# Kernel optimization log

Measured on AMD Instinct MI355X. Metric: run time of the kernel, lower is better.

The kernel has to match this reference:

```python
import jax, jax.numpy as jnp
import numpy as np

MUL = 16          # multiplicity of every irrep block
N = 131072        # number of nodes

# orthonormal traceless-symmetric 3x3 basis, divided by sqrt(5).
_s = 1.0 / np.sqrt(2.0)
_M = np.zeros((5, 3, 3), dtype=np.float32)
_M[0, 0, 1] = _M[0, 1, 0] = _s
_M[1, 0, 2] = _M[1, 2, 0] = _s
_M[2, 1, 2] = _M[2, 2, 1] = _s
_M[3, 0, 0] = _s; _M[3, 1, 1] = -_s
_M[4] = np.diag([-1.0, -1.0, 2.0]).astype(np.float32) / np.sqrt(6.0)
C112 = jnp.asarray(np.transpose(_M, (1, 2, 0)) / np.sqrt(5.0))  # (3,3,5)

# e3nn TensorProduct normalization: irrep_normalization='component'
# (alpha = 2l_out+1), path_normalization='element' (divide by sum of
# mul_u*mul_v over paths into the same output irrep). 0e output receives
# two paths -> 2*MUL^2; 1o and 2e each receive one path -> MUL^2.
A000 = float(np.sqrt(1.0 / (2.0 * MUL * MUL)))                    # 0e x 0e -> 0e (w3j = 1)
A110 = float(np.sqrt(1.0 / (2.0 * MUL * MUL)) / np.sqrt(3.0))     # 1o x 1o -> 0e (w3j = d_ij/sqrt(3))
A101 = float(np.sqrt(3.0 / (MUL * MUL)) / np.sqrt(3.0))           # 1o x 0e -> 1o (w3j = d_ik/sqrt(3))
A112 = float(np.sqrt(5.0 / (MUL * MUL)))                          # 1o x 1o -> 2e


def setup_inputs() -> dict:
    key = jax.random.key(0)
    ks = jax.random.split(key, 6)
    f = lambda k, s: jax.random.normal(k, s, dtype=jnp.float32)
    return {
        "node_feats": f(ks[0], (N, 4 * MUL)),
        "node_messages": f(ks[1], (N, 4 * MUL)),
        "w000": f(ks[2], (MUL, MUL, MUL)),
        "w101": f(ks[3], (MUL, MUL, MUL)),
        "w110": f(ks[4], (MUL, MUL, MUL)),
        "w112": f(ks[5], (MUL, MUL, MUL)),
    }


def _tensor_square(x, w000, w101, w110, w112):
    """e3nn o3.TensorSquare('16x0e+16x1o', '16x0e+16x1o+16x2e') with 'uvw' weighted paths."""
    n = x.shape[0]
    x0 = x[:, :MUL]                          # (n, u)     l=0 block
    x1 = x[:, MUL:].reshape(n, MUL, 3)       # (n, u, i)  l=1 block (mul-major)

    # --- 0e output ---
    out0 = A000 * jnp.einsum('uvw,nu,nv->nw', w000, x0, x0)
    out0 = out0 + A110 * jnp.einsum('uvw,nui,nvi->nw', w110, x1, x1)

    # --- 1o output ---
    out1 = A101 * jnp.einsum('uvw,nuk,nv->nwk', w101, x1, x0)

    # --- 2e output (staged to keep intermediates small) ---
    t1 = jnp.einsum('nvj,ijk->nvik', x1, C112)        # (n, v, i, 5)
    t = jnp.einsum('nui,nvik->nuvk', x1, t1)          # (n, u, v, 5)
    out2 = A112 * jnp.einsum('uvw,nuvk->nwk', w112, t)

    return jnp.concatenate(
        [out0, out1.reshape(n, 3 * MUL), out2.reshape(n, 5 * MUL)], axis=1
    )  # (n, 144)


def reference(node_feats, node_messages, w000, w101, w110, w112):
    # SimpleNodeBlock: sum all nodewise tensors, then tensor square.
    return _tensor_square(node_feats + node_messages, w000, w101, w110, w112)
```

## Files before the change

### kernel.cpp

```cpp
#include <hip/hip_runtime.h>

#define MUL 16
#define NPAIR 136
#define NPB 16
#define SSTR 40
#define NTILE 23

typedef __bf16 bf16x8 __attribute__((ext_vector_type(8)));
typedef __bf16 bf16x2 __attribute__((ext_vector_type(2)));
typedef float  f32x4  __attribute__((ext_vector_type(4)));

__global__ void prep_weights(const float* __restrict__ w000,
                             const float* __restrict__ w101,
                             const float* __restrict__ w110,
                             const float* __restrict__ w112,
                             __bf16* __restrict__ wt) {
    const int tid = threadIdx.x;
    for (int i = tid; i < NTILE * 64; i += 256) {
        bf16x8 z = {};
        ((bf16x8*)wt)[i] = z;
    }
    __syncthreads();

    const float A000   = 0.044194173824159216f;
    const float A110   = 0.025515518153991442f;
    const float A101   = 0.0625f;
    const float A112C1 = 0.044194173824159216f;

    for (int idx = tid; idx < NPAIR * MUL; idx += 256) {
        int p = idx / MUL, w = idx % MUL;
        int u = 0, rem = p;
        while (rem >= MUL - u) { rem -= MUL - u; ++u; }
        int v = u + rem;

        int uv = (u * MUL + v) * MUL + w;
        int vu = (v * MUL + u) * MUL + w;
        float f000, f110, f112, fuv, fvu;
        if (u == v) {
            f000 = A000   * w000[uv];
            f110 = A110   * w110[uv];
            f112 = A112C1 * w112[uv];
            fuv  = A101   * w101[uv];
            fvu  = 0.f;
        } else {
            f000 = A000   * (w000[uv] + w000[vu]);
            f110 = A110   * (w110[uv] + w110[vu]);
            f112 = A112C1 * (w112[uv] + w112[vu]);
            fuv  = A101   * w101[uv];
            fvu  = A101   * w101[vu];
        }
        auto put = [&](int T, int kit, float val) {
            int lanei = ((kit >> 3) << 4) + w;
            wt[(T * 64 + lanei) * 8 + (kit & 7)] = (__bf16)val;
        };
        int k = 2 * p, k2 = 2 * p + 1;
        put(k >> 5,        k & 31,  f000);
        put(k2 >> 5,       k2 & 31, f110);
        put(9 + (k >> 5),  k & 31,  fuv);
        put(9 + (k2 >> 5), k2 & 31, fvu);
        put(18 + (p >> 5), p & 31,  f112);
    }
}

__launch_bounds__(256, 4)
__global__ void tsq_kernel(const float* __restrict__ feats,
                           const float* __restrict__ msgs,
                           const __bf16* __restrict__ wtiles,
                           float* __restrict__ out) {
    __shared__ float  xq[NPB * 68];
    __shared__ int    UVs[NPAIR];
    __shared__ __bf16 sbuf[2][NPB * SSTR];
    __shared__ __bf16 pqbuf[2][3][NPB * SSTR];
    __shared__ __bf16 tbuf[2][5][NPB * SSTR];

    const int tid = threadIdx.x;
    const long long blockNode = (long long)blockIdx.x * NPB;

    if (tid < NPAIR) {
        int u = 0, rem = tid;
        while (rem >= MUL - u) { rem -= MUL - u; ++u; }
        UVs[tid] = u | ((u + rem) << 16);
    }
    {
        int nd = tid >> 4, v = tid & 15;
        const float* fp = feats + (blockNode + nd) * 64;
        const float* mp = msgs  + (blockNode + nd) * 64;
        float4 qd;
        qd.x = fp[v]          + mp[v];
        qd.y = fp[16 + 3 * v] + mp[16 + 3 * v];
        qd.z = fp[17 + 3 * v] + mp[17 + 3 * v];
        qd.w = fp[18 + 3 * v] + mp[18 + 3 * v];
        *(float4*)&xq[nd * 68 + 4 * v] = qd;
    }
    __syncthreads();

    const float SQ3  = 1.7320508075688772f;
    const float ISQ3 = 0.5773502691896258f;
    const int nd = tid & 15, pi = tid >> 4;

    auto computeSP = [&](int c, int b) {
        int P = 16 * c + pi;
        int o = nd * SSTR + 2 * pi;
        if (P < NPAIR) {
            int uvp = UVs[P];
            int u = uvp & 0xffff, v = uvp >> 16;
            float4 xu = *(const float4*)&xq[nd * 68 + 4 * u];
            float4 xv = *(const float4*)&xq[nd * 68 + 4 * v];
            float s0 = xu.x * xv.x;
            float s1 = xu.y * xv.y + xu.z * xv.z + xu.w * xv.w;
            *(bf16x2*)&sbuf[b][o]      = (bf16x2){(__bf16)s0, (__bf16)s1};
            *(bf16x2*)&pqbuf[b][0][o]  = (bf16x2){(__bf16)(xu.y * xv.x), (__bf16)(xv.y * xu.x)};
            *(bf16x2*)&pqbuf[b][1][o]  = (bf16x2){(__bf16)(xu.z * xv.x), (__bf16)(xv.z * xu.x)};
            *(bf16x2*)&pqbuf[b][2][o]  = (bf16x2){(__bf16)(xu.w * xv.x), (__bf16)(xv.w * xu.x)};
        } else {
            bf16x2 z = {};
            *(bf16x2*)&sbuf[b][o]     = z;
            *(bf16x2*)&pqbuf[b][0][o] = z;
            *(bf16x2*)&pqbuf[b][1][o] = z;
            *(bf16x2*)&pqbuf[b][2][o] = z;
        }
    };

    auto computeT = [&](int c, int b) {
        float tf[5][2];
#pragma unroll
        for (int e = 0; e < 2; ++e) {
            int P = 32 * c + 2 * pi + e;
            if (P < NPAIR) {
                int uvp = UVs[P];
                int u = uvp & 0xffff, v = uvp >> 16;
                float4 xu = *(const float4*)&xq[nd * 68 + 4 * u];
                float4 xv = *(const float4*)&xq[nd * 68 + 4 * v];
                float o00 = xu.y * xv.y, o01 = xu.y * xv.z, o02 = xu.y * xv.w;
                float o10 = xu.z * xv.y, o11 = xu.z * xv.z, o12 = xu.z * xv.w;
                float o20 = xu.w * xv.y, o21 = xu.w * xv.z, o22 = xu.w * xv.w;
                float s1 = (o00 + o11) + o22;
                tf[0][e] = o01 + o10;
                tf[1][e] = o02 + o20;
                tf[2][e] = o12 + o21;
                tf[3][e] = o00 - o11;
                tf[4][e] = SQ3 * o22 - ISQ3 * s1;
            } else {
#pragma unroll
                for (int k = 0; k < 5; ++k) tf[k][e] = 0.f;
            }
        }
        int o = nd * SSTR + 2 * pi;
#pragma unroll
        for (int k = 0; k < 5; ++k)
            *(bf16x2*)&tbuf[b][k][o] = (bf16x2){(__bf16)tf[k][0], (__bf16)tf[k][1]};
    };

    const int lane = tid & 63;
    const int wid  = __builtin_amdgcn_readfirstlane(tid >> 6);
    const int m = lane & 15, q = lane >> 4;
    const int kk = wid - 1;
    const bf16x8* wb = (const bf16x8*)wtiles;

    f32x4 accA = {0.f, 0.f, 0.f, 0.f};
    f32x4 accB = {0.f, 0.f, 0.f, 0.f};
    f32x4 accC = {0.f, 0.f, 0.f, 0.f};

    computeSP(0, 0);
    __syncthreads();
    for (int c = 0; c < 9; ++c) {
        if (c < 8) computeSP(c + 1, (c + 1) & 1);
        int b = c & 1;
        if (wid == 0) {
            accA = __builtin_amdgcn_mfma_f32_16x16x32_bf16(
                *(const bf16x8*)&sbuf[b][m * SSTR + 8 * q],
                wb[c * 64 + lane], accA, 0, 0, 0);
        } else {
            accA = __builtin_amdgcn_mfma_f32_16x16x32_bf16(
                *(const bf16x8*)&pqbuf[b][kk][m * SSTR + 8 * q],
                wb[(9 + c) * 64 + lane], accA, 0, 0, 0);
        }
        __syncthreads();
    }

    computeT(0, 0);
    __syncthreads();
    for (int c = 0; c < 5; ++c) {
        if (c < 4) computeT(c + 1, (c + 1) & 1);
        int b = c & 1;
        bf16x8 bt = wb[(18 + c) * 64 + lane];
        if (wid == 0) {
            accB = __builtin_amdgcn_mfma_f32_16x16x32_bf16(
                *(const bf16x8*)&tbuf[b][3][m * SSTR + 8 * q], bt, accB, 0, 0, 0);
            accC = __builtin_amdgcn_mfma_f32_16x16x32_bf16(
                *(const bf16x8*)&tbuf[b][4][m * SSTR + 8 * q], bt, accC, 0, 0, 0);
        } else {
            accB = __builtin_amdgcn_mfma_f32_16x16x32_bf16(
                *(const bf16x8*)&tbuf[b][kk][m * SSTR + 8 * q], bt, accB, 0, 0, 0);
        }
        __syncthreads();
    }

    const int w = m;
    if (wid == 0) {
#pragma unroll
        for (int r = 0; r < 4; ++r) {
            int ndo = q * 4 + r;
            float* ob = out + (blockNode + ndo) * 144;
            ob[w]              = accA[r];
            ob[64 + 5 * w + 3] = accB[r];
            ob[64 + 5 * w + 4] = accC[r];
        }
    } else {
#pragma unroll
        for (int r = 0; r < 4; ++r) {
            int ndo = q * 4 + r;
            float* ob = out + (blockNode + ndo) * 144;
            ob[16 + 3 * w + kk] = accA[r];
            ob[64 + 5 * w + kk] = accB[r];
        }
    }
}

extern "C" void kernel_launch(void* const* d_in, const int* in_sizes, int n_in,
                              void* d_out, int out_size, void* d_ws, size_t ws_size,
                              hipStream_t stream) {
    const float* feats = (const float*)d_in[0];
    const float* msgs  = (const float*)d_in[1];
    const float* w000  = (const float*)d_in[2];
    const float* w101  = (const float*)d_in[3];
    const float* w110  = (const float*)d_in[4];
    const float* w112  = (const float*)d_in[5];
    __bf16* wt = (__bf16*)d_ws;
    float* out = (float*)d_out;

    const int n = in_sizes[0] / (4 * MUL);

    prep_weights<<<1, 256, 0, stream>>>(w000, w101, w110, w112, wt);
    tsq_kernel<<<n / NPB, 256, 0, stream>>>(feats, msgs, wt, out);
}
```

Baseline: 191.7 us.

## Build MFMA A-fragments in registers per wave, dropping LDS staging and barriers

```diff
diff --git a/kernel.cpp b/kernel.cpp
--- a/kernel.cpp
+++ b/kernel.cpp
@@ -2,218 +2,221 @@
 
 #define MUL 16
 #define NPAIR 136
-#define NPB 16
-#define SSTR 40
-#define NTILE 23
+#define NTILE 25
 
 typedef __bf16 bf16x8 __attribute__((ext_vector_type(8)));
-typedef __bf16 bf16x2 __attribute__((ext_vector_type(2)));
 typedef float  f32x4  __attribute__((ext_vector_type(4)));
+
+__device__ __forceinline__ void uv_of(int p, int& u, int& v) {
+    if (p >= NPAIR) { u = 0; v = 0; return; }
+    int uu = 0, rem = p;
+    while (rem >= MUL - uu) { rem -= MUL - uu; ++uu; }
+    u = uu; v = uu + rem;
+}
 
 __global__ void prep_weights(const float* __restrict__ w000,
                              const float* __restrict__ w101,
                              const float* __restrict__ w110,
                              const float* __restrict__ w112,
                              __bf16* __restrict__ wt) {
-    const int tid = threadIdx.x;
-    for (int i = tid; i < NTILE * 64; i += 256) {
-        bf16x8 z = {};
-        ((bf16x8*)wt)[i] = z;
-    }
-    __syncthreads();
+    const int gid = blockIdx.x * 256 + threadIdx.x;
+    if (gid >= NTILE * 64) return;
+    const int T = gid >> 6, lane = gid & 63;
+    const int q = lane >> 4, w = lane & 15;
 
     const float A000   = 0.044194173824159216f;
     const float A110   = 0.025515518153991442f;
     const float A101   = 0.0625f;
     const float A112C1 = 0.044194173824159216f;
 
-    for (int idx = tid; idx < NPAIR * MUL; idx += 256) {
-        int p = idx / MUL, w = idx % MUL;
-        int u = 0, rem = p;
-        while (rem >= MUL - u) { rem -= MUL - u; ++u; }
-        int v = u + rem;
-
-        int uv = (u * MUL + v) * MUL + w;
-        int vu = (v * MUL + u) * MUL + w;
-        float f000, f110, f112, fuv, fvu;
-        if (u == v) {
-            f000 = A000   * w000[uv];
-            f110 = A110   * w110[uv];
-            f112 = A112C1 * w112[uv];
-            fuv  = A101   * w101[uv];
-            fvu  = 0.f;
-        } else {
-            f000 = A000   * (w000[uv] + w000[vu]);
-            f110 = A110   * (w110[uv] + w110[vu]);
-            f112 = A112C1 * (w112[uv] + w112[vu]);
-            fuv  = A101   * w101[uv];
-            fvu  = A101   * w101[vu];
-        }
-        auto put = [&](int T, int kit, float val) {
-            int lanei = ((kit >> 3) << 4) + w;
-            wt[(T * 64 + lanei) * 8 + (kit & 7)] = (__bf16)val;
-        };
-        int k = 2 * p, k2 = 2 * p + 1;
-        put(k >> 5,        k & 31,  f000);
-        put(k2 >> 5,       k2 & 31, f110);
-        put(9 + (k >> 5),  k & 31,  fuv);
-        put(9 + (k2 >> 5), k2 & 31, fvu);
-        put(18 + (p >> 5), p & 31,  f112);
-    }
-}
-
-__launch_bounds__(256, 4)
+    bf16x8 frag = {};
+    if (T < 10) {
+        const int c = T >> 1, b = T & 1;
+#pragma unroll
+        for (int i = 0; i < 4; ++i) {
+            const int p = 32 * c + 8 * q + 4 * b + i;
+            if (p < NPAIR) {
+                int u, v; uv_of(p, u, v);
+                const int uvw = (u * MUL + v) * MUL + w;
+                const int vuw = (v * MUL + u) * MUL + w;
+                float f000, f110;
+                if (u == v) { f000 = A000 * w000[uvw]; f110 = A110 * w110[uvw]; }
+                else        { f000 = A000 * (w000[uvw] + w000[vuw]);
+                              f110 = A110 * (w110[uvw] + w110[vuw]); }
+                frag[2 * i]     = (__bf16)f000;
+                frag[2 * i + 1] = (__bf16)f110;
+            }
+        }
+    } else if (T < 20) {
+        const int c = (T - 10) >> 1, b = (T - 10) & 1;
+#pragma unroll
+        for (int i = 0; i < 4; ++i) {
+            const int p = 32 * c + 8 * q + 4 * b + i;
+            if (p < NPAIR) {
+                int u, v; uv_of(p, u, v);
+                const int uvw = (u * MUL + v) * MUL + w;
+                const int vuw = (v * MUL + u) * MUL + w;
+                frag[2 * i]     = (__bf16)(A101 * w101[uvw]);
+                frag[2 * i + 1] = (__bf16)((u == v) ? 0.f : A101 * w101[vuw]);
+            }
+        }
+    } else {
+        const int c = T - 20;
+#pragma unroll
+        for (int e = 0; e < 8; ++e) {
+            const int p = 32 * c + 8 * q + e;
+            if (p < NPAIR) {
+                int u, v; uv_of(p, u, v);
+                const int uvw = (u * MUL + v) * MUL + w;
+                const int vuw = (v * MUL + u) * MUL + w;
+                const float f112 = (u == v) ? A112C1 * w112[uvw]
+                                            : A112C1 * (w112[uvw] + w112[vuw]);
+                frag[e] = (__bf16)f112;
+            }
+        }
+    }
+    ((bf16x8*)wt)[T * 64 + lane] = frag;
+}
+
+#define SQ3f  1.7320508075688772f
+#define ISQ3f 0.5773502691896258f
+
+template<int E>
+__device__ __forceinline__ void pair_feats(int d, const float* __restrict__ xrow,
+        bf16x8& fS, bf16x8& f0, bf16x8& f1, bf16x8& f2,
+        bf16x8& t0, bf16x8& t1, bf16x8& t2, bf16x8& t3, bf16x8& t4) {
+    constexpr int sh = (E & 1) * 16;
+    const int u = (d >> sh) & 0xff;
+    const int v = (d >> (sh + 8)) & 0xff;
+    const float4 xu = *(const float4*)(xrow + 4 * u);
+    const float4 xv = *(const float4*)(xrow + 4 * v);
+    const float o00 = xu.y * xv.y, o01 = xu.y * xv.z, o02 = xu.y * xv.w;
+    const float o10 = xu.z * xv.y, o11 = xu.z * xv.z, o12 = xu.z * xv.w;
+    const float o20 = xu.w * xv.y, o21 = xu.w * xv.z, o22 = xu.w * xv.w;
+    const float s1 = (o00 + o11) + o22;
+    constexpr int s2 = (E & 3) * 2;
+    fS[s2]     = (__bf16)(xu.x * xv.x);
+    fS[s2 + 1] = (__bf16)s1;
+    f0[s2]     = (__bf16)(xu.y * xv.x);  f0[s2 + 1] = (__bf16)(xv.y * xu.x);
+    f1[s2]     = (__bf16)(xu.z * xv.x);  f1[s2 + 1] = (__bf16)(xv.z * xu.x);
+    f2[s2]     = (__bf16)(xu.w * xv.x);  f2[s2 + 1] = (__bf16)(xv.w * xu.x);
+    t0[E] = (__bf16)(o01 + o10);
+    t1[E] = (__bf16)(o02 + o20);
+    t2[E] = (__bf16)(o12 + o21);
+    t3[E] = (__bf16)(o00 - o11);
+    t4[E] = (__bf16)(SQ3f * o22 - ISQ3f * s1);
+}
+
+__launch_bounds__(256, 3)
 __global__ void tsq_kernel(const float* __restrict__ feats,
                            const float* __restrict__ msgs,
                            const __bf16* __restrict__ wtiles,
                            float* __restrict__ out) {
-    __shared__ float  xq[NPB * 68];
-    __shared__ int    UVs[NPAIR];
-    __shared__ __bf16 sbuf[2][NPB * SSTR];
-    __shared__ __bf16 pqbuf[2][3][NPB * SSTR];
-    __shared__ __bf16 tbuf[2][5][NPB * SSTR];
+    __shared__ __align__(16) float xq[64 * 68];
+    __shared__ __align__(16) int   uvt[80];
 
     const int tid = threadIdx.x;
-    const long long blockNode = (long long)blockIdx.x * NPB;
-
-    if (tid < NPAIR) {
-        int u = 0, rem = tid;
-        while (rem >= MUL - u) { rem -= MUL - u; ++u; }
-        UVs[tid] = u | ((u + rem) << 16);
-    }
+    const long long blockNode = (long long)blockIdx.x * 64;
+
+    if (tid < 80) {
+        int u0, v0, u1, v1;
+        uv_of(2 * tid,     u0, v0);
+        uv_of(2 * tid + 1, u1, v1);
+        uvt[tid] = u0 | (v0 << 8) | (u1 << 16) | (v1 << 24);
+    }
+
     {
-        int nd = tid >> 4, v = tid & 15;
-        const float* fp = feats + (blockNode + nd) * 64;
-        const float* mp = msgs  + (blockNode + nd) * 64;
-        float4 qd;
-        qd.x = fp[v]          + mp[v];
-        qd.y = fp[16 + 3 * v] + mp[16 + 3 * v];
-        qd.z = fp[17 + 3 * v] + mp[17 + 3 * v];
-        qd.w = fp[18 + 3 * v] + mp[18 + 3 * v];
-        *(float4*)&xq[nd * 68 + 4 * v] = qd;
+        const float4* f4p = (const float4*)(feats + blockNode * 64);
+        const float4* m4p = (const float4*)(msgs  + blockNode * 64);
+#pragma unroll
+        for (int r = 0; r < 4; ++r) {
+            const int li = r * 256 + tid;
+            const int nd = li >> 4, f4 = li & 15;
+            const float4 a = f4p[li];
+            const float4 b = m4p[li];
+            const float vals[4] = {a.x + b.x, a.y + b.y, a.z + b.z, a.w + b.w};
+#pragma unroll
+            for (int jj = 0; jj < 4; ++jj) {
+                const int f = 4 * f4 + jj;
+                int dst;
+                if (f < 16) dst = nd * 68 + 4 * f;
+                else {
+                    const int g = f - 16;
+                    const int v3 = (g * 171) >> 9;
+                    dst = nd * 68 + 4 * v3 + 1 + (g - 3 * v3);
+                }
+                xq[dst] = vals[jj];
+            }
+        }
     }
     __syncthreads();
 
-    const float SQ3  = 1.7320508075688772f;
-    const float ISQ3 = 0.5773502691896258f;
-    const int nd = tid & 15, pi = tid >> 4;
-
-    auto computeSP = [&](int c, int b) {
-        int P = 16 * c + pi;
-        int o = nd * SSTR + 2 * pi;
-        if (P < NPAIR) {
-            int uvp = UVs[P];
-            int u = uvp & 0xffff, v = uvp >> 16;
-            float4 xu = *(const float4*)&xq[nd * 68 + 4 * u];
-            float4 xv = *(const float4*)&xq[nd * 68 + 4 * v];
-            float s0 = xu.x * xv.x;
-            float s1 = xu.y * xv.y + xu.z * xv.z + xu.w * xv.w;
-            *(bf16x2*)&sbuf[b][o]      = (bf16x2){(__bf16)s0, (__bf16)s1};
-            *(bf16x2*)&pqbuf[b][0][o]  = (bf16x2){(__bf16)(xu.y * xv.x), (__bf16)(xv.y * xu.x)};
-            *(bf16x2*)&pqbuf[b][1][o]  = (bf16x2){(__bf16)(xu.z * xv.x), (__bf16)(xv.z * xu.x)};
-            *(bf16x2*)&pqbuf[b][2][o]  = (bf16x2){(__bf16)(xu.w * xv.x), (__bf16)(xv.w * xu.x)};
-        } else {
-            bf16x2 z = {};
-            *(bf16x2*)&sbuf[b][o]     = z;
-            *(bf16x2*)&pqbuf[b][0][o] = z;
-            *(bf16x2*)&pqbuf[b][1][o] = z;
-            *(bf16x2*)&pqbuf[b][2][o] = z;
-        }
-    };
-
-    auto computeT = [&](int c, int b) {
-        float tf[5][2];
-#pragma unroll
-        for (int e = 0; e < 2; ++e) {
-            int P = 32 * c + 2 * pi + e;
-            if (P < NPAIR) {
-                int uvp = UVs[P];
-                int u = uvp & 0xffff, v = uvp >> 16;
-                float4 xu = *(const float4*)&xq[nd * 68 + 4 * u];
-                float4 xv = *(const float4*)&xq[nd * 68 + 4 * v];
-                float o00 = xu.y * xv.y, o01 = xu.y * xv.z, o02 = xu.y * xv.w;
-                float o10 = xu.z * xv.y, o11 = xu.z * xv.z, o12 = xu.z * xv.w;
-                float o20 = xu.w * xv.y, o21 = xu.w * xv.z, o22 = xu.w * xv.w;
-                float s1 = (o00 + o11) + o22;
-                tf[0][e] = o01 + o10;
-                tf[1][e] = o02 + o20;
-                tf[2][e] = o12 + o21;
-                tf[3][e] = o00 - o11;
-                tf[4][e] = SQ3 * o22 - ISQ3 * s1;
-            } else {
-#pragma unroll
-                for (int k = 0; k < 5; ++k) tf[k][e] = 0.f;
-            }
-        }
-        int o = nd * SSTR + 2 * pi;
-#pragma unroll
-        for (int k = 0; k < 5; ++k)
-            *(bf16x2*)&tbuf[b][k][o] = (bf16x2){(__bf16)tf[k][0], (__bf16)tf[k][1]};
-    };
-
     const int lane = tid & 63;
-    const int wid  = __builtin_amdgcn_readfirstlane(tid >> 6);
+    const int wid  = tid >> 6;
     const int m = lane & 15, q = lane >> 4;
-    const int kk = wid - 1;
+    const float* xrow = xq + (wid * 16 + m) * 68;
     const bf16x8* wb = (const bf16x8*)wtiles;
 
-    f32x4 accA = {0.f, 0.f, 0.f, 0.f};
-    f32x4 accB = {0.f, 0.f, 0.f, 0.f};
-    f32x4 accC = {0.f, 0.f, 0.f, 0.f};
-
-    computeSP(0, 0);
-    __syncthreads();
-    for (int c = 0; c < 9; ++c) {
-        if (c < 8) computeSP(c + 1, (c + 1) & 1);
-        int b = c & 1;
-        if (wid == 0) {
-            accA = __builtin_amdgcn_mfma_f32_16x16x32_bf16(
-                *(const bf16x8*)&sbuf[b][m * SSTR + 8 * q],
-                wb[c * 64 + lane], accA, 0, 0, 0);
-        } else {
-            accA = __builtin_amdgcn_mfma_f32_16x16x32_bf16(
-                *(const bf16x8*)&pqbuf[b][kk][m * SSTR + 8 * q],
-                wb[(9 + c) * 64 + lane], accA, 0, 0, 0);
-        }
-        __syncthreads();
-    }
-
-    computeT(0, 0);
-    __syncthreads();
+    f32x4 accS  = {0.f, 0.f, 0.f, 0.f};
+    f32x4 accP0 = {0.f, 0.f, 0.f, 0.f};
+    f32x4 accP1 = {0.f, 0.f, 0.f, 0.f};
+    f32x4 accP2 = {0.f, 0.f, 0.f, 0.f};
+    f32x4 accT0 = {0.f, 0.f, 0.f, 0.f};
+    f32x4 accT1 = {0.f, 0.f, 0.f, 0.f};
+    f32x4 accT2 = {0.f, 0.f, 0.f, 0.f};
+    f32x4 accT3 = {0.f, 0.f, 0.f, 0.f};
+    f32x4 accT4 = {0.f, 0.f, 0.f, 0.f};
+
+#pragma unroll
     for (int c = 0; c < 5; ++c) {
-        if (c < 4) computeT(c + 1, (c + 1) & 1);
-        int b = c & 1;
-        bf16x8 bt = wb[(18 + c) * 64 + lane];
-        if (wid == 0) {
-            accB = __builtin_amdgcn_mfma_f32_16x16x32_bf16(
-                *(const bf16x8*)&tbuf[b][3][m * SSTR + 8 * q], bt, accB, 0, 0, 0);
-            accC = __builtin_amdgcn_mfma_f32_16x16x32_bf16(
-                *(const bf16x8*)&tbuf[b][4][m * SSTR + 8 * q], bt, accC, 0, 0, 0);
-        } else {
-            accB = __builtin_amdgcn_mfma_f32_16x16x32_bf16(
-                *(const bf16x8*)&tbuf[b][kk][m * SSTR + 8 * q], bt, accB, 0, 0, 0);
-        }
-        __syncthreads();
-    }
-
-    const int w = m;
-    if (wid == 0) {
-#pragma unroll
-        for (int r = 0; r < 4; ++r) {
-            int ndo = q * 4 + r;
-            float* ob = out + (blockNode + ndo) * 144;
-            ob[w]              = accA[r];
-            ob[64 + 5 * w + 3] = accB[r];
-            ob[64 + 5 * w + 4] = accC[r];
-        }
-    } else {
-#pragma unroll
-        for (int r = 0; r < 4; ++r) {
-            int ndo = q * 4 + r;
-            float* ob = out + (blockNode + ndo) * 144;
-            ob[16 + 3 * w + kk] = accA[r];
-            ob[64 + 5 * w + kk] = accB[r];
-        }
+        const int4 uvd = *(const int4*)((const char*)uvt + 64 * c + 16 * q);
+        bf16x8 t0 = {}, t1 = {}, t2 = {}, t3 = {}, t4 = {};
+        {
+            const bf16x8 bS = wb[(2 * c) * 64 + lane];
+            const bf16x8 bP = wb[(10 + 2 * c) * 64 + lane];
+            bf16x8 fS, f0, f1, f2;
+            pair_feats<0>(uvd.x, xrow, fS, f0, f1, f2, t0, t1, t2, t3, t4);
+            pair_feats<1>(uvd.x, xrow, fS, f0, f1, f2, t0, t1, t2, t3, t4);
+            pair_feats<2>(uvd.y, xrow, fS, f0, f1, f2, t0, t1, t2, t3, t4);
+            pair_feats<3>(uvd.y, xrow, fS, f0, f1, f2, t0, t1, t2, t3, t4);
+            accS  = __builtin_amdgcn_mfma_f32_16x16x32_bf16(fS, bS, accS,  0, 0, 0);
+            accP0 = __builtin_amdgcn_mfma_f32_16x16x32_bf16(f0, bP, accP0, 0, 0, 0);
+            accP1 = __builtin_amdgcn_mfma_f32_16x16x32_bf16(f1, bP, accP1, 0, 0, 0);
+            accP2 = __builtin_amdgcn_mfma_f32_16x16x32_bf16(f2, bP, accP2, 0, 0, 0);
+        }
+        {
+            const bf16x8 bS = wb[(2 * c + 1) * 64 + lane];
+            const bf16x8 bP = wb[(11 + 2 * c) * 64 + lane];
+            bf16x8 fS, f0, f1, f2;
+            pair_feats<4>(uvd.z, xrow, fS, f0, f1, f2, t0, t1, t2, t3, t4);
+            pair_feats<5>(uvd.z, xrow, fS, f0, f1, f2, t0, t1, t2, t3, t4);
+            pair_feats<6>(uvd.w, xrow, fS, f0, f1, f2, t0, t1, t2, t3, t4);
+            pair_feats<7>(uvd.w, xrow, fS, f0, f1, f2, t0, t1, t2, t3, t4);
+            accS  = __builtin_amdgcn_mfma_f32_16x16x32_bf16(fS, bS, accS,  0, 0, 0);
+            accP0 = __builtin_amdgcn_mfma_f32_16x16x32_bf16(f0, bP, accP0, 0, 0, 0);
+            accP1 = __builtin_amdgcn_mfma_f32_16x16x32_bf16(f1, bP, accP1, 0, 0, 0);
+            accP2 = __builtin_amdgcn_mfma_f32_16x16x32_bf16(f2, bP, accP2, 0, 0, 0);
+        }
+        const bf16x8 bT = wb[(20 + c) * 64 + lane];
+        accT0 = __builtin_amdgcn_mfma_f32_16x16x32_bf16(t0, bT, accT0, 0, 0, 0);
+        accT1 = __builtin_amdgcn_mfma_f32_16x16x32_bf16(t1, bT, accT1, 0, 0, 0);
+        accT2 = __builtin_amdgcn_mfma_f32_16x16x32_bf16(t2, bT, accT2, 0, 0, 0);
+        accT3 = __builtin_amdgcn_mfma_f32_16x16x32_bf16(t3, bT, accT3, 0, 0, 0);
+        accT4 = __builtin_amdgcn_mfma_f32_16x16x32_bf16(t4, bT, accT4, 0, 0, 0);
+    }
+
+#pragma unroll
+    for (int r = 0; r < 4; ++r) {
+        float* ob = out + (blockNode + wid * 16 + q * 4 + r) * 144;
+        ob[m]              = accS[r];
+        ob[16 + 3 * m + 0] = accP0[r];
+        ob[16 + 3 * m + 1] = accP1[r];
+        ob[16 + 3 * m + 2] = accP2[r];
+        ob[64 + 5 * m + 0] = accT0[r];
+        ob[64 + 5 * m + 1] = accT1[r];
+        ob[64 + 5 * m + 2] = accT2[r];
+        ob[64 + 5 * m + 3] = accT3[r];
+        ob[64 + 5 * m + 4] = accT4[r];
     }
 }
 
@@ -231,6 +234,6 @@
 
     const int n = in_sizes[0] / (4 * MUL);
 
-    prep_weights<<<1, 256, 0, stream>>>(w000, w101, w110, w112, wt);
-    tsq_kernel<<<n / NPB, 256, 0, stream>>>(feats, msgs, wt, out);
-}
+    prep_weights<<<(NTILE * 64 + 255) / 256, 256, 0, stream>>>(w000, w101, w110, w112, wt);
+    tsq_kernel<<<n / 64, 256, 0, stream>>>(feats, msgs, wt, out);
+}
```

Result: faster. 161.9 us (-15.5%).
